# Kernel tuning notes

Measured on AMD Instinct MI355X. Metric: run time of the kernel, lower is better.

The kernel has to match this reference:

```python
import jax, jax.numpy as jnp
import numpy as np

N_NODES = 100000
N_EDGES = 1600000


def setup_inputs() -> dict:
    key = jax.random.key(0)
    k1, k2, k3, k4 = jax.random.split(key, 4)
    x = jax.random.normal(k1, (N_NODES, 128), dtype=jnp.float32)
    edge_index = jax.random.randint(k2, (2, N_EDGES), 0, N_NODES, dtype=jnp.int64)
    # Glorot-ish init for weights
    W1 = jax.random.normal(k3, (128, 128), dtype=jnp.float32) * (1.0 / np.sqrt(128))
    b1 = jnp.zeros((128,), dtype=jnp.float32)
    W2 = jax.random.normal(k4, (128, 64), dtype=jnp.float32) * (1.0 / np.sqrt(128))
    b2 = jnp.zeros((64,), dtype=jnp.float32)
    return {"x": x, "edge_index": edge_index, "W1": W1, "b1": b1, "W2": W2, "b2": b2}


def _gcn_conv(x, src, dst, W, b):
    """PyG GCNConv: h = W x; symmetric deg^-1/2 norm over edges (incl. self-loops); scatter-add; + bias."""
    n = x.shape[0]
    h = x @ W  # [N, out]
    ones = jnp.ones(src.shape[0], dtype=h.dtype)
    deg = jax.ops.segment_sum(ones, dst, num_segments=n)  # in-degree incl self-loops
    dinv = jax.lax.rsqrt(jnp.maximum(deg, 1e-12))
    norm = dinv[src] * dinv[dst]  # [E+N]
    msg = h[src] * norm[:, None]  # [E+N, out] gather
    out = jax.ops.segment_sum(msg, dst, num_segments=n)  # scatter-add
    return out + b


def reference(x, edge_index, W1, b1, W2, b2):
    n = x.shape[0]
    loop = jnp.arange(n, dtype=edge_index.dtype)
    src = jnp.concatenate([edge_index[0], loop])  # add self-loops
    dst = jnp.concatenate([edge_index[1], loop])
    h = jax.nn.relu(_gcn_conv(x, src, dst, W1, b1))
    # dropout is identity in eval mode
    return _gcn_conv(h, src, dst, W2, b2)
```

## Files before the change

kernel.cpp:

```cpp
#include <hip/hip_runtime.h>
#include <hip/hip_bf16.h>

#define THREADS 256
#define BSHIFT 9
#define BIN_CHUNK 4096
#define KP 136

typedef __attribute__((ext_vector_type(8))) short bf16x8;
typedef __attribute__((ext_vector_type(8))) unsigned short u16x8;
typedef __attribute__((ext_vector_type(4))) float f32x4;


__device__ inline unsigned short f2bf(float f) {
    unsigned int u = __float_as_uint(f);
    unsigned int r = (u + 0x7fffu + ((u >> 16) & 1u)) >> 16;
    return (unsigned short)r;
}

__device__ inline float2 bf2_to_f2(unsigned int u) {
    float2 r;
    r.x = __uint_as_float(u << 16);
    r.y = __uint_as_float(u & 0xffff0000u);
    return r;
}

__device__ inline void accum_row(float* acc, uint4 v) {
    float2 a = bf2_to_f2(v.x), b = bf2_to_f2(v.y), c = bf2_to_f2(v.z), d = bf2_to_f2(v.w);
    acc[0] += a.x; acc[1] += a.y; acc[2] += b.x; acc[3] += b.y;
    acc[4] += c.x; acc[5] += c.y; acc[6] += d.x; acc[7] += d.y;
}

__device__ inline void accum_row_scaled(float* acc, uint4 v, float s) {
    float2 a = bf2_to_f2(v.x), b = bf2_to_f2(v.y), c = bf2_to_f2(v.z), d = bf2_to_f2(v.w);
    acc[0] = fmaf(s, a.x, acc[0]); acc[1] = fmaf(s, a.y, acc[1]);
    acc[2] = fmaf(s, b.x, acc[2]); acc[3] = fmaf(s, b.y, acc[3]);
    acc[4] = fmaf(s, c.x, acc[4]); acc[5] = fmaf(s, c.y, acc[5]);
    acc[6] = fmaf(s, d.x, acc[6]); acc[7] = fmaf(s, d.y, acc[7]);
}

__device__ inline bf16x8 load_bfrag(const float* __restrict__ W, int ldn, int k0, int col) {
    bf16x8 b;
#pragma unroll
    for (int i = 0; i < 8; ++i) b[i] = (short)f2bf(W[(size_t)(k0 + i) * ldn + col]);
    return b;
}


__global__ __launch_bounds__(256) void k_bin_gemm1(const int* __restrict__ src,
                                                   const int* __restrict__ dst,
                                                   int* __restrict__ bcur,
                                                   unsigned int* __restrict__ binned,
                                                   int E, int NB, int cap,
                                                   const float* __restrict__ x,
                                                   const float* __restrict__ W1,
                                                   unsigned short* __restrict__ h,
                                                   int M, int nbin) {
    __shared__ __align__(16) short As[64 * KP];
    const int t = threadIdx.x;

    if ((int)blockIdx.x < nbin) {
        int* bcnt = (int*)As;
        int* bres = bcnt + 256;
        bcnt[t] = 0;
        __syncthreads();
        int base = blockIdx.x * BIN_CHUNK;
        int sv[16], dv[16];
#pragma unroll
        for (int i = 0; i < 16; ++i) {
            int e = base + t + i * 256;
            if (e < E) {
                sv[i] = src[e];
                dv[i] = dst[e];
                atomicAdd(&bcnt[dv[i] >> BSHIFT], 1);
            } else {
                dv[i] = -1;
            }
        }
        __syncthreads();
        if (t < NB) {
            int old = bcnt[t] ? atomicAdd(&bcur[t], bcnt[t]) : 0;
            bres[t] = t * cap + old;
        }
        __syncthreads();
#pragma unroll
        for (int i = 0; i < 16; ++i) {
            if (dv[i] >= 0) {
                int b = dv[i] >> BSHIFT;
                int pos = atomicAdd(&bres[b], 1);
                if (pos < (b + 1) * cap)
                    binned[pos] = ((unsigned int)(dv[i] & 511) << 23) | (unsigned int)sv[i];
            }
        }
        return;
    }

    const int m0 = ((int)blockIdx.x - nbin) * 64;
    {
        int ar = t >> 5;
        int ac = (t & 31) * 4;
#pragma unroll
        for (int rb = 0; rb < 64; rb += 8) {
            int lrow = rb + ar;
            int row = m0 + lrow;
            ushort4 sv = make_ushort4(0, 0, 0, 0);
            if (row < M) {
                float4 v = *(const float4*)(x + (size_t)row * 128 + ac);
                sv.x = f2bf(v.x); sv.y = f2bf(v.y); sv.z = f2bf(v.z); sv.w = f2bf(v.w);
            }
            *(ushort4*)&As[lrow * KP + ac] = sv;
        }
    }
    __syncthreads();

    const int w = t >> 6;
    const int lane = t & 63;
    const int lm = lane & 15;
    const int qd = lane >> 4;
    const int n0w = w * 32;

    f32x4 acc[4][2];
#pragma unroll
    for (int mi = 0; mi < 4; ++mi)
#pragma unroll
        for (int ni = 0; ni < 2; ++ni) acc[mi][ni] = (f32x4){0.f, 0.f, 0.f, 0.f};

#pragma unroll
    for (int ks = 0; ks < 4; ++ks) {
        bf16x8 b0 = load_bfrag(W1, 128, ks * 32 + qd * 8, n0w + lm);
        bf16x8 b1 = load_bfrag(W1, 128, ks * 32 + qd * 8, n0w + 16 + lm);
#pragma unroll
        for (int mi = 0; mi < 4; ++mi) {
            bf16x8 a = *(const bf16x8*)&As[(mi * 16 + lm) * KP + ks * 32 + qd * 8];
            acc[mi][0] = __builtin_amdgcn_mfma_f32_16x16x32_bf16(a, b0, acc[mi][0], 0, 0, 0);
            acc[mi][1] = __builtin_amdgcn_mfma_f32_16x16x32_bf16(a, b1, acc[mi][1], 0, 0, 0);
        }
    }

#pragma unroll
    for (int mi = 0; mi < 4; ++mi) {
#pragma unroll
        for (int ni = 0; ni < 2; ++ni) {
            int col = n0w + ni * 16 + lm;
#pragma unroll
            for (int r = 0; r < 4; ++r) {
                int lrow = mi * 16 + qd * 4 + r;
                int row = m0 + lrow;
                if (row < M) h[(size_t)row * 128 + col] = f2bf(acc[mi][ni][r]);
            }
        }
    }
}

__global__ __launch_bounds__(256) void k_node_place(const unsigned int* __restrict__ binned,
                                                    const int* __restrict__ bcur, int cap,
                                                    int* __restrict__ rp,
                                                    int* __restrict__ deg,
                                                    float* __restrict__ dinv,
                                                    int* __restrict__ eperm, int N,
                                                    const float* __restrict__ W2,
                                                    unsigned short* __restrict__ W2t, int NB) {
    int b = blockIdx.x;
    int t = threadIdx.x;
    if (b == NB) {
        for (int i = t; i < 64 * 128; i += 256) {
            int nn = i >> 7;
            int kk = i & 127;
            W2t[i] = f2bf(W2[(size_t)kk * 64 + nn]);
        }
        return;
    }
    __shared__ int lc[512];
    __shared__ int s[256];
    int beg = b * cap;
    int end = beg + min(bcur[b], cap);
    int d0 = b << BSHIFT;
    lc[t] = 0;
    lc[t + 256] = 0;
    __syncthreads();
    for (int j = beg + t; j < end; j += 256) atomicAdd(&lc[binned[j] >> 23], 1);
    __syncthreads();
    int a = lc[2 * t], c = lc[2 * t + 1];
    int pair = a + c;
    s[t] = pair;
    __syncthreads();
    for (int off = 1; off < 256; off <<= 1) {
        int add = (t >= off) ? s[t - off] : 0;
        __syncthreads();
        s[t] += add;
        __syncthreads();
    }
    int excl = s[t] - pair;
    int st0 = beg + excl, st1 = st0 + a;
    int node0 = d0 + 2 * t;
    if (node0 < N) {
        rp[node0] = st0;
        deg[node0] = a;
        dinv[node0] = rsqrtf((float)a + 1.0f);
    }
    if (node0 + 1 < N) {
        rp[node0 + 1] = st1;
        deg[node0 + 1] = c;
        dinv[node0 + 1] = rsqrtf((float)c + 1.0f);
    }
    __syncthreads();
    lc[2 * t] = st0;
    lc[2 * t + 1] = st1;
    __syncthreads();
    for (int j = beg + t; j < end; j += 256) {
        unsigned int p = binned[j];
        int pos = atomicAdd(&lc[p >> 23], 1);
        eperm[pos] = (int)(p & 0x7fffffu);
    }
}


__global__ __launch_bounds__(256) void k_gather_gemm2(const int* __restrict__ rp,
                                                      const int* __restrict__ deg,
                                                      const int* __restrict__ eperm,
                                                      const float* __restrict__ dinv,
                                                      const uint4* __restrict__ h4,
                                                      const float* __restrict__ b1,
                                                      const unsigned short* __restrict__ W2t,
                                                      unsigned short* __restrict__ h2,
                                                      int n) {
    __shared__ __align__(16) short As[16 * KP];

    const int t = threadIdx.x;
    const int lane = t & 63;
    const int l16 = lane & 15;
    const int gbase = lane & 48;
    const int m0 = blockIdx.x * 16;
    const int lrow = (t >> 6) * 4 + (lane >> 4);
    const int node = m0 + lrow;
    const bool valid = node < n;

    int beg = 0, end = 0;
    float dv_self = 0.f;
    if (valid) {
        beg = rp[node];
        end = beg + deg[node];
        dv_self = dinv[node];
    }

    float acc[8];
#pragma unroll
    for (int i = 0; i < 8; ++i) acc[i] = 0.f;
    if (valid) accum_row_scaled(acc, h4[(size_t)node * 16 + l16], dv_self);

    for (int j = beg; j < end; j += 16) {
        int cnt = end - j;
        if (cnt > 16) cnt = 16;
        int ep = eperm[j + (l16 < cnt ? l16 : cnt - 1)];
        float dvv = dinv[ep];
        int k = 0;
        for (; k + 4 <= cnt; k += 4) {
            int i0 = __shfl(ep, gbase + k);
            int i1 = __shfl(ep, gbase + k + 1);
            int i2 = __shfl(ep, gbase + k + 2);
            int i3 = __shfl(ep, gbase + k + 3);
            float d0 = __shfl(dvv, gbase + k);
            float d1 = __shfl(dvv, gbase + k + 1);
            float d2 = __shfl(dvv, gbase + k + 2);
            float d3 = __shfl(dvv, gbase + k + 3);
            uint4 v0 = h4[(size_t)i0 * 16 + l16];
            uint4 v1 = h4[(size_t)i1 * 16 + l16];
            uint4 v2 = h4[(size_t)i2 * 16 + l16];
            uint4 v3 = h4[(size_t)i3 * 16 + l16];
            accum_row_scaled(acc, v0, d0);
            accum_row_scaled(acc, v1, d1);
            accum_row_scaled(acc, v2, d2);
            accum_row_scaled(acc, v3, d3);
        }
        for (; k < cnt; ++k) {
            int i0 = __shfl(ep, gbase + k);
            float d0 = __shfl(dvv, gbase + k);
            uint4 v0 = h4[(size_t)i0 * 16 + l16];
            accum_row_scaled(acc, v0, d0);
        }
    }

    {
        float4 bb0 = ((const float4*)b1)[l16 * 2];
        float4 bb1 = ((const float4*)b1)[l16 * 2 + 1];
        u16x8 s;
        s[0] = f2bf(fmaxf(fmaf(dv_self, acc[0], bb0.x), 0.f));
        s[1] = f2bf(fmaxf(fmaf(dv_self, acc[1], bb0.y), 0.f));
        s[2] = f2bf(fmaxf(fmaf(dv_self, acc[2], bb0.z), 0.f));
        s[3] = f2bf(fmaxf(fmaf(dv_self, acc[3], bb0.w), 0.f));
        s[4] = f2bf(fmaxf(fmaf(dv_self, acc[4], bb1.x), 0.f));
        s[5] = f2bf(fmaxf(fmaf(dv_self, acc[5], bb1.y), 0.f));
        s[6] = f2bf(fmaxf(fmaf(dv_self, acc[6], bb1.z), 0.f));
        s[7] = f2bf(fmaxf(fmaf(dv_self, acc[7], bb1.w), 0.f));
        *(u16x8*)&As[lrow * KP + l16 * 8] = s;
    }
    __syncthreads();

    const int w = t >> 6;
    const int lm = lane & 15;
    const int qd = lane >> 4;
    const int col = w * 16 + lm;

    f32x4 c4 = (f32x4){0.f, 0.f, 0.f, 0.f};
#pragma unroll
    for (int ks = 0; ks < 4; ++ks) {
        bf16x8 b = *(const bf16x8*)&W2t[(size_t)col * 128 + ks * 32 + qd * 8];
        bf16x8 a = *(const bf16x8*)&As[lm * KP + ks * 32 + qd * 8];
        c4 = __builtin_amdgcn_mfma_f32_16x16x32_bf16(a, b, c4, 0, 0, 0);
    }

#pragma unroll
    for (int r = 0; r < 4; ++r) {
        int row = m0 + qd * 4 + r;
        if (row < n) h2[(size_t)row * 64 + col] = f2bf(dinv[row] * c4[r]);
    }
}

__global__ __launch_bounds__(256) void k_gather64(const int* __restrict__ rp,
                                                  const int* __restrict__ deg,
                                                  const int* __restrict__ eperm,
                                                  const float* __restrict__ dinv,
                                                  const uint4* __restrict__ h4,
                                                  const float* __restrict__ bias,
                                                  float* __restrict__ out, int n) {
    const int t = threadIdx.x;
    const int lane = t & 63;
    const int l8 = lane & 7;
    const int gbase = lane & 56;
    const int node = blockIdx.x * 32 + (t >> 6) * 8 + (lane >> 3);
    const bool valid = node < n;

    int beg = 0, end = 0;
    if (valid) {
        beg = rp[node];
        end = beg + deg[node];
    }

    float acc[8];
#pragma unroll
    for (int i = 0; i < 8; ++i) acc[i] = 0.f;
    if (valid) accum_row(acc, h4[(size_t)node * 8 + l8]);

    int j = beg;
    for (; j + 16 <= end; j += 16) {
        int ep0 = eperm[j + l8];
        int ep1 = eperm[j + 8 + l8];
        int idx[16];
#pragma unroll
        for (int k = 0; k < 8; ++k) idx[k] = __shfl(ep0, gbase + k);
#pragma unroll
        for (int k = 0; k < 8; ++k) idx[8 + k] = __shfl(ep1, gbase + k);
        uint4 v[16];
#pragma unroll
        for (int k = 0; k < 16; ++k) v[k] = h4[(size_t)idx[k] * 8 + l8];
#pragma unroll
        for (int k = 0; k < 16; ++k) accum_row(acc, v[k]);
    }
    int cnt = end - j;
    if (cnt >= 8) {
        int ep = eperm[j + l8];
        int idx[8];
#pragma unroll
        for (int k = 0; k < 8; ++k) idx[k] = __shfl(ep, gbase + k);
        uint4 v[8];
#pragma unroll
        for (int k = 0; k < 8; ++k) v[k] = h4[(size_t)idx[k] * 8 + l8];
#pragma unroll
        for (int k = 0; k < 8; ++k) accum_row(acc, v[k]);
        j += 8;
        cnt -= 8;
    }
    if (cnt > 0) {
        int ep = eperm[j + (l8 < cnt ? l8 : cnt - 1)];
        int k = 0;
        for (; k + 4 <= cnt; k += 4) {
            int i0 = __shfl(ep, gbase + k);
            int i1 = __shfl(ep, gbase + k + 1);
            int i2 = __shfl(ep, gbase + k + 2);
            int i3 = __shfl(ep, gbase + k + 3);
            uint4 v0 = h4[(size_t)i0 * 8 + l8];
            uint4 v1 = h4[(size_t)i1 * 8 + l8];
            uint4 v2 = h4[(size_t)i2 * 8 + l8];
            uint4 v3 = h4[(size_t)i3 * 8 + l8];
            accum_row(acc, v0);
            accum_row(acc, v1);
            accum_row(acc, v2);
            accum_row(acc, v3);
        }
        for (; k < cnt; ++k) {
            int i0 = __shfl(ep, gbase + k);
            uint4 v0 = h4[(size_t)i0 * 8 + l8];
            accum_row(acc, v0);
        }
    }

    if (valid) {
        float dv = dinv[node];
        float4 b0 = ((const float4*)bias)[l8 * 2];
        float4 b1 = ((const float4*)bias)[l8 * 2 + 1];
        float4 o0, o1;
        o0.x = dv * acc[0] + b0.x; o0.y = dv * acc[1] + b0.y;
        o0.z = dv * acc[2] + b0.z; o0.w = dv * acc[3] + b0.w;
        o1.x = dv * acc[4] + b1.x; o1.y = dv * acc[5] + b1.y;
        o1.z = dv * acc[6] + b1.z; o1.w = dv * acc[7] + b1.w;
        float4* orow = (float4*)(out + (size_t)node * 64);
        orow[l8 * 2] = o0;
        orow[l8 * 2 + 1] = o1;
    }
}


extern "C" void kernel_launch(void* const* d_in, const int* in_sizes, int n_in,
                              void* d_out, int out_size, void* d_ws, size_t ws_size,
                              hipStream_t stream) {
    const float* x  = (const float*)d_in[0];
    const int*   ei = (const int*)d_in[1];
    const float* W1 = (const float*)d_in[2];
    const float* b1 = (const float*)d_in[3];
    const float* W2 = (const float*)d_in[4];
    const float* b2 = (const float*)d_in[5];
    float* out = (float*)d_out;

    const int N = in_sizes[0] / 128;
    const int E = in_sizes[1] / 2;
    const int* src = ei;
    const int* dst = ei + E;
    const int NB = (N + 511) >> BSHIFT;
    const int cap = (E + NB - 1) / NB + ((E / NB) >> 2) + 1024;

    char* ws = (char*)d_ws;
    size_t off = 0;
    auto carve = [&](size_t bytes) -> void* {
        void* p = ws + off;
        off = (off + bytes + 255) & ~(size_t)255;
        return p;
    };
    float* dinv = (float*)carve((size_t)N * 4);
    int*   rp   = (int*)carve((size_t)N * 4);
    int*   deg  = (int*)carve((size_t)N * 4);
    int*   bcur = (int*)carve(256 * 4);
    unsigned int* binned = (unsigned int*)carve((size_t)NB * cap * 4);
    int*   eperm = (int*)carve((size_t)NB * cap * 4);
    unsigned short* h   = (unsigned short*)carve((size_t)N * 128 * 2);
    unsigned short* h2  = (unsigned short*)carve((size_t)N * 64 * 2);
    unsigned short* W2t = (unsigned short*)carve(64 * 128 * 2);

    const int gMm = (N + 63) / 64;
    const int nbin = (E + BIN_CHUNK - 1) / BIN_CHUNK;

    hipMemsetAsync(bcur, 0, 256 * sizeof(int), stream);
    k_bin_gemm1<<<nbin + gMm, THREADS, 0, stream>>>(src, dst, bcur, binned, E, NB, cap,
                                                    x, W1, h, N, nbin);
    k_node_place<<<NB + 1, THREADS, 0, stream>>>(binned, bcur, cap, rp, deg, dinv, eperm, N,
                                                 W2, W2t, NB);

    k_gather_gemm2<<<(N + 15) / 16, THREADS, 0, stream>>>(rp, deg, eperm, dinv, (const uint4*)h,
                                                          b1, W2t, h2, N);

    k_gather64<<<(N + 31) / 32, THREADS, 0, stream>>>(rp, deg, eperm, dinv, (const uint4*)h2, b2, out, N);
}
```

Measured before the change: 258.0 us.

## Pack fp16 source dinv into edge permutation to avoid per-edge dinv gathers

The global in-degree array is now computed with atomics during binning. The placement kernel looks up each source node's dinv, converts it to fp16 and packs it into the upper 15 bits of the eperm entry alongside a 17-bit source index. The first gather kernel decodes the scale from the packed word, removing a dependent random dinv load and a shuffle per edge. The cost is a global atomic per edge, a random deg read during placement, lower precision for the normalisation, and a hard 131072-node limit on the index field.

```diff
diff --git a/kernel.cpp b/kernel.cpp
--- a/kernel.cpp
+++ b/kernel.cpp
@@ -1,10 +1,12 @@
 #include <hip/hip_runtime.h>
 #include <hip/hip_bf16.h>
+#include <hip/hip_fp16.h>
 
 #define THREADS 256
 #define BSHIFT 9
 #define BIN_CHUNK 4096
 #define KP 136
+#define SRCMASK 0x1ffff
 
 typedef __attribute__((ext_vector_type(8))) short bf16x8;
 typedef __attribute__((ext_vector_type(8))) unsigned short u16x8;
@@ -38,6 +40,10 @@
     acc[6] = fmaf(s, d.x, acc[6]); acc[7] = fmaf(s, d.y, acc[7]);
 }
 
+__device__ inline float ep_dinv(int ep) {
+    return __half2float(__ushort_as_half((unsigned short)((unsigned int)ep >> 17)));
+}
+
 __device__ inline bf16x8 load_bfrag(const float* __restrict__ W, int ldn, int k0, int col) {
     bf16x8 b;
 #pragma unroll
@@ -49,6 +55,7 @@
 __global__ __launch_bounds__(256) void k_bin_gemm1(const int* __restrict__ src,
                                                    const int* __restrict__ dst,
                                                    int* __restrict__ bcur,
+                                                   int* __restrict__ deg,
                                                    unsigned int* __restrict__ binned,
                                                    int E, int NB, int cap,
                                                    const float* __restrict__ x,
@@ -72,6 +79,7 @@
                 sv[i] = src[e];
                 dv[i] = dst[e];
                 atomicAdd(&bcnt[dv[i] >> BSHIFT], 1);
+                atomicAdd(&deg[dv[i]], 1);
             } else {
                 dv[i] = -1;
             }
@@ -154,7 +162,7 @@
 __global__ __launch_bounds__(256) void k_node_place(const unsigned int* __restrict__ binned,
                                                     const int* __restrict__ bcur, int cap,
                                                     int* __restrict__ rp,
-                                                    int* __restrict__ deg,
+                                                    const int* __restrict__ deg,
                                                     float* __restrict__ dinv,
                                                     int* __restrict__ eperm, int N,
                                                     const float* __restrict__ W2,
@@ -194,12 +202,10 @@
     int node0 = d0 + 2 * t;
     if (node0 < N) {
         rp[node0] = st0;
-        deg[node0] = a;
         dinv[node0] = rsqrtf((float)a + 1.0f);
     }
     if (node0 + 1 < N) {
         rp[node0 + 1] = st1;
-        deg[node0 + 1] = c;
         dinv[node0 + 1] = rsqrtf((float)c + 1.0f);
     }
     __syncthreads();
@@ -208,8 +214,11 @@
     __syncthreads();
     for (int j = beg + t; j < end; j += 256) {
         unsigned int p = binned[j];
+        int srcn = (int)(p & 0x7fffffu);
+        float dv = rsqrtf((float)deg[srcn] + 1.0f);
+        unsigned int hb = (unsigned int)__half_as_ushort(__float2half(dv));
         int pos = atomicAdd(&lc[p >> 23], 1);
-        eperm[pos] = (int)(p & 0x7fffffu);
+        eperm[pos] = (int)((unsigned int)srcn | (hb << 17));
     }
 }
 
@@ -251,31 +260,25 @@
         int cnt = end - j;
         if (cnt > 16) cnt = 16;
         int ep = eperm[j + (l16 < cnt ? l16 : cnt - 1)];
-        float dvv = dinv[ep];
         int k = 0;
         for (; k + 4 <= cnt; k += 4) {
-            int i0 = __shfl(ep, gbase + k);
-            int i1 = __shfl(ep, gbase + k + 1);
-            int i2 = __shfl(ep, gbase + k + 2);
-            int i3 = __shfl(ep, gbase + k + 3);
-            float d0 = __shfl(dvv, gbase + k);
-            float d1 = __shfl(dvv, gbase + k + 1);
-            float d2 = __shfl(dvv, gbase + k + 2);
-            float d3 = __shfl(dvv, gbase + k + 3);
-            uint4 v0 = h4[(size_t)i0 * 16 + l16];
-            uint4 v1 = h4[(size_t)i1 * 16 + l16];
-            uint4 v2 = h4[(size_t)i2 * 16 + l16];
-            uint4 v3 = h4[(size_t)i3 * 16 + l16];
-            accum_row_scaled(acc, v0, d0);
-            accum_row_scaled(acc, v1, d1);
-            accum_row_scaled(acc, v2, d2);
-            accum_row_scaled(acc, v3, d3);
+            int e0 = __shfl(ep, gbase + k);
+            int e1 = __shfl(ep, gbase + k + 1);
+            int e2 = __shfl(ep, gbase + k + 2);
+            int e3 = __shfl(ep, gbase + k + 3);
+            uint4 v0 = h4[(size_t)(e0 & SRCMASK) * 16 + l16];
+            uint4 v1 = h4[(size_t)(e1 & SRCMASK) * 16 + l16];
+            uint4 v2 = h4[(size_t)(e2 & SRCMASK) * 16 + l16];
+            uint4 v3 = h4[(size_t)(e3 & SRCMASK) * 16 + l16];
+            accum_row_scaled(acc, v0, ep_dinv(e0));
+            accum_row_scaled(acc, v1, ep_dinv(e1));
+            accum_row_scaled(acc, v2, ep_dinv(e2));
+            accum_row_scaled(acc, v3, ep_dinv(e3));
         }
         for (; k < cnt; ++k) {
-            int i0 = __shfl(ep, gbase + k);
-            float d0 = __shfl(dvv, gbase + k);
-            uint4 v0 = h4[(size_t)i0 * 16 + l16];
-            accum_row_scaled(acc, v0, d0);
+            int e0 = __shfl(ep, gbase + k);
+            uint4 v0 = h4[(size_t)(e0 & SRCMASK) * 16 + l16];
+            accum_row_scaled(acc, v0, ep_dinv(e0));
         }
     }
 
@@ -342,8 +345,8 @@
 
     int j = beg;
     for (; j + 16 <= end; j += 16) {
-        int ep0 = eperm[j + l8];
-        int ep1 = eperm[j + 8 + l8];
+        int ep0 = eperm[j + l8] & SRCMASK;
+        int ep1 = eperm[j + 8 + l8] & SRCMASK;
         int idx[16];
 #pragma unroll
         for (int k = 0; k < 8; ++k) idx[k] = __shfl(ep0, gbase + k);
@@ -357,7 +360,7 @@
     }
     int cnt = end - j;
     if (cnt >= 8) {
-        int ep = eperm[j + l8];
+        int ep = eperm[j + l8] & SRCMASK;
         int idx[8];
 #pragma unroll
         for (int k = 0; k < 8; ++k) idx[k] = __shfl(ep, gbase + k);
@@ -370,7 +373,7 @@
         cnt -= 8;
     }
     if (cnt > 0) {
-        int ep = eperm[j + (l8 < cnt ? l8 : cnt - 1)];
+        int ep = eperm[j + (l8 < cnt ? l8 : cnt - 1)] & SRCMASK;
         int k = 0;
         for (; k + 4 <= cnt; k += 4) {
             int i0 = __shfl(ep, gbase + k);
@@ -434,10 +437,10 @@
         off = (off + bytes + 255) & ~(size_t)255;
         return p;
     };
+    int*   bcur = (int*)carve(256 * 4);
+    int*   deg  = (int*)carve((size_t)N * 4);
     float* dinv = (float*)carve((size_t)N * 4);
     int*   rp   = (int*)carve((size_t)N * 4);
-    int*   deg  = (int*)carve((size_t)N * 4);
-    int*   bcur = (int*)carve(256 * 4);
     unsigned int* binned = (unsigned int*)carve((size_t)NB * cap * 4);
     int*   eperm = (int*)carve((size_t)NB * cap * 4);
     unsigned short* h   = (unsigned short*)carve((size_t)N * 128 * 2);
@@ -447,8 +450,8 @@
     const int gMm = (N + 63) / 64;
     const int nbin = (E + BIN_CHUNK - 1) / BIN_CHUNK;
 
-    hipMemsetAsync(bcur, 0, 256 * sizeof(int), stream);
-    k_bin_gemm1<<<nbin + gMm, THREADS, 0, stream>>>(src, dst, bcur, binned, E, NB, cap,
+    hipMemsetAsync(bcur, 0, 256 * 4 + (size_t)N * 4, stream);
+    k_bin_gemm1<<<nbin + gMm, THREADS, 0, stream>>>(src, dst, bcur, deg, binned, E, NB, cap,
                                                     x, W1, h, N, nbin);
     k_node_place<<<NB + 1, THREADS, 0, stream>>>(binned, bcur, cap, rp, deg, dinv, eperm, N,
                                                  W2, W2t, NB);
```

Result: slower. 304.4 us (+18.0%).
